# Performance work log

Hardware: AMD Instinct MI355X
Metric: run time of the kernel (lower is better)

The kernel has to match this reference:

```python
import jax, jax.numpy as jnp
import numpy as np

B, C, P, D = 4096, 1000, 10, 256
N = C * P            # total prototypes
E = 160000           # edges among prototypes
MARGIN = -0.1
LOSS_WEIGHT = 0.1
EPS = 1e-12          # F.normalize eps


def _gcn_conv(x, src, dst, deg_isqrt, w, b):
    # PyG GCNConv: symmetric-normalized aggregation with self-loops (added by caller)
    xw = x @ w                                   # [N, D]
    norm = deg_isqrt[src] * deg_isqrt[dst]       # [E+N]
    msg = norm[:, None] * xw[src]                # [E+N, D]
    out = jax.ops.segment_sum(msg, dst, num_segments=N)
    return out + b


def setup_inputs() -> dict:
    key = jax.random.key(0)
    ks = jax.random.split(key, 8)
    return {
        "hidden": jax.random.normal(ks[0], (B, D), jnp.float32),
        "labels": jax.random.randint(ks[1], (B,), 0, C),
        "edge_index": jax.random.randint(ks[2], (2, E), 0, N),
        "node_features": 0.02 * jax.random.normal(ks[3], (N, D), jnp.float32),
        "w1": jax.random.normal(ks[4], (D, D), jnp.float32) / np.sqrt(D),
        "b1": jnp.zeros((D,), jnp.float32),
        "w2": jax.random.normal(ks[5], (D, D), jnp.float32) / np.sqrt(D),
        "b2": jnp.zeros((D,), jnp.float32),
    }


def reference(hidden, labels, edge_index, node_features, w1, b1, w2, b2):
    # --- PrototypeGCN over the prototype graph (self-loops + sym norm) ---
    loops = jnp.arange(N, dtype=edge_index.dtype)
    src = jnp.concatenate([edge_index[0], loops])
    dst = jnp.concatenate([edge_index[1], loops])
    deg = jax.ops.segment_sum(jnp.ones_like(dst, jnp.float32), dst, num_segments=N)
    deg_isqrt = jnp.where(deg > 0, jax.lax.rsqrt(jnp.maximum(deg, 1.0)), 0.0)
    x = node_features
    x = jax.nn.relu(_gcn_conv(x, src, dst, deg_isqrt, w1, b1))
    x = jax.nn.relu(_gcn_conv(x, src, dst, deg_isqrt, w2, b2))

    # --- cosine similarity, per-class max over prototypes ---
    hidden_norm = hidden / jnp.maximum(jnp.linalg.norm(hidden, axis=1, keepdims=True), EPS)
    proto_norm = x / jnp.maximum(jnp.linalg.norm(x, axis=1, keepdims=True), EPS)
    sim = (1.0 + hidden_norm @ proto_norm.T) / 2.0          # [B, N]
    sim_pc = sim.reshape(B, C, P)
    output = sim_pc.max(axis=2)                              # [B, C]
    topk_idx = sim_pc.argmax(axis=2)                         # [B, C]

    # --- margin-masked cross entropy ---
    ar = jnp.arange(B)
    true_scores = output[ar, labels]
    pred_labels = output.argmax(axis=1)
    pred_scores = output.max(axis=1)
    mask = (true_scores - pred_scores) > MARGIN              # [B] bool
    cnt = mask.sum()
    per_ce = -jax.nn.log_softmax(output, axis=1)[ar, labels]
    ce_loss = jnp.sum(per_ce * mask) / jnp.maximum(cnt, 1).astype(per_ce.dtype)

    # dispersion = -mean(proto_norm @ proto_norm.T) = -||sum_i p_i||^2 / N^2
    s = proto_norm.sum(axis=0)
    dispersion_loss = -(s @ s) / (N * N)
    total_loss = jnp.where(cnt == 0, 0.0, ce_loss + LOSS_WEIGHT * dispersion_loss)

    # --- vectorized usage scatter (replaces Python double loop) ---
    pos_ids = labels * P + topk_idx[ar, labels]
    positive_usage = jnp.zeros((N,), jnp.float32).at[pos_ids].add(1.0)
    wrong = (pred_labels != labels).astype(jnp.float32)
    neg_ids = pred_labels * P + topk_idx[ar, pred_labels]
    negative_usage = jnp.zeros((N,), jnp.float32).at[neg_ids].add(wrong)

    return (output, total_loss, positive_usage, negative_usage)
```

## Files before the change

kernel.cpp:

```cpp
#include <hip/hip_runtime.h>
#include <math.h>

#define B_  4096
#define C_  1000
#define P_  10
#define D_  256
#define N_  10000
#define E_  160000

typedef __attribute__((ext_vector_type(8))) short short8;
typedef __attribute__((ext_vector_type(4))) float floatx4;

#define MFMA16(a, b, c) __builtin_amdgcn_mfma_f32_16x16x32_bf16((a), (b), (c), 0, 0, 0)

__device__ __forceinline__ float waveReduceSum(float v){
  #pragma unroll
  for (int o = 32; o > 0; o >>= 1) v += __shfl_xor(v, o);
  return v;
}
__device__ __forceinline__ unsigned short f2bf(float f){
  unsigned int u = __float_as_uint(f);
  unsigned int r = (u + 0x7FFFu + ((u >> 16) & 1u)) >> 16;
  return (unsigned short)r;
}
__device__ __forceinline__ float bf2f(unsigned short b){
  return __uint_as_float(((unsigned int)b) << 16);
}
__device__ __forceinline__ void gload_lds16(const void* g, void* l){
  __builtin_amdgcn_global_load_lds((const __attribute__((address_space(1))) void*)g,
                                   (__attribute__((address_space(3))) void*)l, 16, 0, 0);
}
__device__ __forceinline__ void split8(const float* __restrict__ p, short8& h8, short8& l8){
  float4 v0 = *(const float4*)p;
  float4 v1 = *(const float4*)(p + 4);
  float v[8] = {v0.x, v0.y, v0.z, v0.w, v1.x, v1.y, v1.z, v1.w};
  #pragma unroll
  for (int j = 0; j < 8; ++j){
    unsigned short h = f2bf(v[j]);
    h8[j] = (short)h;
    l8[j] = (short)f2bf(v[j] - bf2f(h));
  }
}

__global__ void k_prep(const int* __restrict__ src, const int* __restrict__ dst,
                       int* __restrict__ cursor, int* __restrict__ csr_src,
                       const float* __restrict__ w1, const float* __restrict__ w2,
                       unsigned short* __restrict__ w1h, unsigned short* __restrict__ w1l,
                       unsigned short* __restrict__ w2h, unsigned short* __restrict__ w2l,
                       float* __restrict__ zero_zone){
  int b = blockIdx.x;
  if (b < 625){
    int e = b * 256 + threadIdx.x;
    if (e < E_){
      int d = dst[e];
      int p = atomicAdd(&cursor[d], 1);
      p = (p < 63) ? p : 63;
      csr_src[d * 64 + p] = src[e];
    }
  } else if (b < 1137){
    int bb = b - 625;
    int k = threadIdx.x;
    const float* w = (bb < 256) ? w1 : w2;
    int n = bb & 255;
    float x = w[(size_t)k * 256 + n];
    unsigned short h = f2bf(x);
    unsigned short l = f2bf(x - bf2f(h));
    if (bb < 256){ w1h[(size_t)n * 256 + k] = h; w1l[(size_t)n * 256 + k] = l; }
    else         { w2h[(size_t)n * 256 + k] = h; w2l[(size_t)n * 256 + k] = l; }
  } else {
    int i = (b - 1137) * 256 + threadIdx.x;
    if (i < 1 + 2 * N_) zero_zone[i] = 0.f;
  }
}

__global__ __launch_bounds__(64) void k_gemm_mfma(
    const float* __restrict__ A,
    const unsigned short* __restrict__ Wh, const unsigned short* __restrict__ Wl,
    float* __restrict__ outp){
  int lane = threadIdx.x;
  int l15 = lane & 15, lq = lane >> 4;
  int rb = blockIdx.x * 64;
  int nb = blockIdx.y * 32;

  floatx4 acc[4][2];
  #pragma unroll
  for (int mt = 0; mt < 4; ++mt)
    #pragma unroll
    for (int nt = 0; nt < 2; ++nt) acc[mt][nt] = (floatx4){0.f,0.f,0.f,0.f};

  int arow[4];
  #pragma unroll
  for (int mt = 0; mt < 4; ++mt){
    int r = rb + mt * 16 + l15;
    arow[mt] = (r < N_) ? r : (N_ - 1);
  }
  for (int kc = 0; kc < 256; kc += 32){
    short8 ah[4], al[4], bh[2], bl[2];
    #pragma unroll
    for (int mt = 0; mt < 4; ++mt)
      split8(A + (size_t)arow[mt] * 256 + kc + lq * 8, ah[mt], al[mt]);
    #pragma unroll
    for (int nt = 0; nt < 2; ++nt){
      size_t o = (size_t)(nb + nt * 16 + l15) * 256 + kc + lq * 8;
      bh[nt] = *(const short8*)(Wh + o);
      bl[nt] = *(const short8*)(Wl + o);
    }
    #pragma unroll
    for (int nt = 0; nt < 2; ++nt)
      #pragma unroll
      for (int mt = 0; mt < 4; ++mt) acc[mt][nt] = MFMA16(al[mt], bh[nt], acc[mt][nt]);
    #pragma unroll
    for (int nt = 0; nt < 2; ++nt)
      #pragma unroll
      for (int mt = 0; mt < 4; ++mt) acc[mt][nt] = MFMA16(ah[mt], bl[nt], acc[mt][nt]);
    #pragma unroll
    for (int nt = 0; nt < 2; ++nt)
      #pragma unroll
      for (int mt = 0; mt < 4; ++mt) acc[mt][nt] = MFMA16(ah[mt], bh[nt], acc[mt][nt]);
  }
  #pragma unroll
  for (int mt = 0; mt < 4; ++mt)
    #pragma unroll
    for (int r = 0; r < 4; ++r){
      int row = rb + mt * 16 + lq * 4 + r;
      if (row < N_){
        #pragma unroll
        for (int nt = 0; nt < 2; ++nt)
          outp[(size_t)row * 256 + nb + nt * 16 + l15] = acc[mt][nt][r];
      }
    }
}

__global__ void k_agg_relu(const float* __restrict__ XW, const int* __restrict__ deg,
                           const int* __restrict__ csr_src,
                           const float* __restrict__ bias, float* __restrict__ X1){
  int n    = blockIdx.x * 4 + (threadIdx.x >> 6);
  int lane = threadIdx.x & 63;
  int c4   = lane * 4;
  int dgn = deg[n];
  int dg = (dgn < 64) ? dgn : 64;
  int   esr = (lane < dg) ? csr_src[n * 64 + lane] : 0;
  float is  = 1.0f / sqrtf((float)(dgn + 1));
  float en  = (1.0f / sqrtf((float)(deg[esr] + 1))) * is;
  float4 s = *(const float4*)(XW + (size_t)n * 256 + c4);
  float w = is * is;
  float4 a = make_float4(w * s.x, w * s.y, w * s.z, w * s.w);
  int i = 0;
  for (; i + 3 < dg; i += 4){
    int s0 = __shfl(esr, i),   s1 = __shfl(esr, i+1), s2 = __shfl(esr, i+2), s3 = __shfl(esr, i+3);
    float n0 = __shfl(en, i),  n1 = __shfl(en, i+1),  n2 = __shfl(en, i+2),  n3 = __shfl(en, i+3);
    float4 v0 = *(const float4*)(XW + (size_t)s0 * 256 + c4);
    float4 v1 = *(const float4*)(XW + (size_t)s1 * 256 + c4);
    float4 v2 = *(const float4*)(XW + (size_t)s2 * 256 + c4);
    float4 v3 = *(const float4*)(XW + (size_t)s3 * 256 + c4);
    a.x += n0*v0.x + n1*v1.x + n2*v2.x + n3*v3.x;
    a.y += n0*v0.y + n1*v1.y + n2*v2.y + n3*v3.y;
    a.z += n0*v0.z + n1*v1.z + n2*v2.z + n3*v3.z;
    a.w += n0*v0.w + n1*v1.w + n2*v2.w + n3*v3.w;
  }
  for (; i < dg; ++i){
    int s0 = __shfl(esr, i); float n0 = __shfl(en, i);
    float4 v0 = *(const float4*)(XW + (size_t)s0 * 256 + c4);
    a.x += n0 * v0.x; a.y += n0 * v0.y; a.z += n0 * v0.z; a.w += n0 * v0.w;
  }
  float4 b = *(const float4*)(bias + c4);
  float4 o;
  o.x = fmaxf(a.x + b.x, 0.f); o.y = fmaxf(a.y + b.y, 0.f);
  o.z = fmaxf(a.z + b.z, 0.f); o.w = fmaxf(a.w + b.w, 0.f);
  *(float4*)(X1 + (size_t)n * 256 + c4) = o;
}

__global__ void k_agg_norm_split(const float* __restrict__ XW, const int* __restrict__ deg,
                                 const int* __restrict__ csr_src,
                                 const float* __restrict__ bias,
                                 unsigned short* __restrict__ Ph, unsigned short* __restrict__ Pl){
  int n    = blockIdx.x * 4 + (threadIdx.x >> 6);
  int lane = threadIdx.x & 63;
  int c4   = lane * 4;
  int dgn = deg[n];
  int dg = (dgn < 64) ? dgn : 64;
  int   esr = (lane < dg) ? csr_src[n * 64 + lane] : 0;
  float is  = 1.0f / sqrtf((float)(dgn + 1));
  float en  = (1.0f / sqrtf((float)(deg[esr] + 1))) * is;
  float4 s = *(const float4*)(XW + (size_t)n * 256 + c4);
  float w = is * is;
  float4 a = make_float4(w * s.x, w * s.y, w * s.z, w * s.w);
  int i = 0;
  for (; i + 3 < dg; i += 4){
    int s0 = __shfl(esr, i),   s1 = __shfl(esr, i+1), s2 = __shfl(esr, i+2), s3 = __shfl(esr, i+3);
    float n0 = __shfl(en, i),  n1 = __shfl(en, i+1),  n2 = __shfl(en, i+2),  n3 = __shfl(en, i+3);
    float4 v0 = *(const float4*)(XW + (size_t)s0 * 256 + c4);
    float4 v1 = *(const float4*)(XW + (size_t)s1 * 256 + c4);
    float4 v2 = *(const float4*)(XW + (size_t)s2 * 256 + c4);
    float4 v3 = *(const float4*)(XW + (size_t)s3 * 256 + c4);
    a.x += n0*v0.x + n1*v1.x + n2*v2.x + n3*v3.x;
    a.y += n0*v0.y + n1*v1.y + n2*v2.y + n3*v3.y;
    a.z += n0*v0.z + n1*v1.z + n2*v2.z + n3*v3.z;
    a.w += n0*v0.w + n1*v1.w + n2*v2.w + n3*v3.w;
  }
  for (; i < dg; ++i){
    int s0 = __shfl(esr, i); float n0 = __shfl(en, i);
    float4 v0 = *(const float4*)(XW + (size_t)s0 * 256 + c4);
    a.x += n0 * v0.x; a.y += n0 * v0.y; a.z += n0 * v0.z; a.w += n0 * v0.w;
  }
  float4 b = *(const float4*)(bias + c4);
  float x0 = fmaxf(a.x + b.x, 0.f), x1 = fmaxf(a.y + b.y, 0.f);
  float x2 = fmaxf(a.z + b.z, 0.f), x3 = fmaxf(a.w + b.w, 0.f);
  float ss = x0*x0 + x1*x1 + x2*x2 + x3*x3;
  float tot = waveReduceSum(ss);
  float nrm = fmaxf(sqrtf(tot), 1e-12f);
  x0 /= nrm; x1 /= nrm; x2 /= nrm; x3 /= nrm;
  unsigned short h0 = f2bf(x0), h1 = f2bf(x1), h2 = f2bf(x2), h3 = f2bf(x3);
  ushort4 hv = make_ushort4(h0, h1, h2, h3);
  ushort4 lv = make_ushort4(f2bf(x0 - bf2f(h0)), f2bf(x1 - bf2f(h1)),
                            f2bf(x2 - bf2f(h2)), f2bf(x3 - bf2f(h3)));
  *(ushort4*)(Ph + (size_t)n * 256 + c4) = hv;
  *(ushort4*)(Pl + (size_t)n * 256 + c4) = lv;
}

__global__ void k_norm_split(const float* __restrict__ in,
                             unsigned short* __restrict__ hi,
                             unsigned short* __restrict__ lo,
                             const unsigned short* __restrict__ Ph,
                             const unsigned short* __restrict__ Pl,
                             float* __restrict__ svec){
  int r = blockIdx.x, t = threadIdx.x;
  if (r < B_){
    float v = in[(size_t)r * 256 + t];
    float ss = waveReduceSum(v * v);
    __shared__ float red[4];
    int w = t >> 6;
    if ((t & 63) == 0) red[w] = ss;
    __syncthreads();
    float tot = red[0] + red[1] + red[2] + red[3];
    float nrm = fmaxf(sqrtf(tot), 1e-12f);
    float x = v / nrm;
    unsigned short h = f2bf(x);
    unsigned short l = f2bf(x - bf2f(h));
    hi[(size_t)r * 256 + t] = h;
    lo[(size_t)r * 256 + t] = l;
  } else {
    int r0 = (r - B_) * 100;
    float acc = 0.f;
    for (int rr = r0; rr < r0 + 100; ++rr)
      acc += bf2f(Ph[(size_t)rr * 256 + t]) + bf2f(Pl[(size_t)rr * 256 + t]);
    atomicAdd(&svec[t], acc);
  }
}

__global__ __launch_bounds__(256, 4) void k_sim_max(
    const unsigned short* __restrict__ HNh, const unsigned short* __restrict__ HNl,
    const unsigned short* __restrict__ PNh, const unsigned short* __restrict__ PNl,
    float* __restrict__ out, unsigned char* __restrict__ idxb){
  __shared__ __align__(16) char smem[20736];

  int tid  = threadIdx.x;
  int wid  = tid >> 6;
  int lane = tid & 63;
  int l15  = lane & 15, lq = lane >> 4;
  int rbw  = blockIdx.y * 128 + wid * 32;
  int cb80 = blockIdx.x * 80;

  int swz  = (l15 >> 1) & 3;
  int srow = lane >> 2;
  int skq  = (lane & 3) ^ ((lane >> 3) & 3);

  floatx4 acc[2][5];
  #pragma unroll
  for (int mt = 0; mt < 2; ++mt)
    #pragma unroll
    for (int nt = 0; nt < 5; ++nt) acc[mt][nt] = (floatx4){0.f,0.f,0.f,0.f};

  const unsigned short* a0h = HNh + (size_t)(rbw + l15) * 256 + lq * 8;
  const unsigned short* a0l = HNl + (size_t)(rbw + l15) * 256 + lq * 8;

  auto stage1 = [&](int kc, int pb, int c){
    int bsel = (c >= 5) ? 1 : 0;
    int s = c - bsel * 5;
    int row = s * 16 + srow;
    const unsigned short* gp = (bsel ? PNl : PNh)
        + (size_t)(cb80 + row) * 256 + kc + skq * 8;
    char* lp = smem + pb * 10240 + bsel * 5120 + s * 1024;
    gload_lds16(gp, lp);
  };
  auto stageAll = [&](int kc, int pb){
    stage1(kc, pb, wid);
    stage1(kc, pb, wid + 4);
    if (wid < 2) stage1(kc, pb, wid + 8);
  };

  stageAll(0, 0);
  short8 ah[2], al[2];
  #pragma unroll
  for (int mt = 0; mt < 2; ++mt){
    ah[mt] = *(const short8*)(a0h + (size_t)mt * 4096);
    al[mt] = *(const short8*)(a0l + (size_t)mt * 4096);
  }
  __syncthreads();

  int p = 0;
  for (int kc = 0; kc < 256; kc += 32){
    const unsigned short* Bh = (const unsigned short*)(smem + p * 10240);
    const unsigned short* Bl = Bh + 2560;
    short8 ah2[2], al2[2];
    if (kc < 224){
      stageAll(kc + 32, p ^ 1);
      #pragma unroll
      for (int mt = 0; mt < 2; ++mt){
        ah2[mt] = *(const short8*)(a0h + (size_t)mt * 4096 + kc + 32);
        al2[mt] = *(const short8*)(a0l + (size_t)mt * 4096 + kc + 32);
      }
    }
    {
      int r0 = (0 * 16 + l15) * 32 + (lq ^ swz) * 8;
      int r1 = (1 * 16 + l15) * 32 + (lq ^ swz) * 8;
      int r2 = (2 * 16 + l15) * 32 + (lq ^ swz) * 8;
      short8 bh0 = *(const short8*)(Bh + r0), bl0 = *(const short8*)(Bl + r0);
      short8 bh1 = *(const short8*)(Bh + r1), bl1 = *(const short8*)(Bl + r1);
      short8 bh2 = *(const short8*)(Bh + r2), bl2 = *(const short8*)(Bl + r2);
      acc[0][0] = MFMA16(al[0], bh0, acc[0][0]);
      acc[1][0] = MFMA16(al[1], bh0, acc[1][0]);
      acc[0][1] = MFMA16(al[0], bh1, acc[0][1]);
      acc[1][1] = MFMA16(al[1], bh1, acc[1][1]);
      acc[0][2] = MFMA16(al[0], bh2, acc[0][2]);
      acc[1][2] = MFMA16(al[1], bh2, acc[1][2]);
      acc[0][0] = MFMA16(ah[0], bl0, acc[0][0]);
      acc[1][0] = MFMA16(ah[1], bl0, acc[1][0]);
      acc[0][1] = MFMA16(ah[0], bl1, acc[0][1]);
      acc[1][1] = MFMA16(ah[1], bl1, acc[1][1]);
      acc[0][2] = MFMA16(ah[0], bl2, acc[0][2]);
      acc[1][2] = MFMA16(ah[1], bl2, acc[1][2]);
      acc[0][0] = MFMA16(ah[0], bh0, acc[0][0]);
      acc[1][0] = MFMA16(ah[1], bh0, acc[1][0]);
      acc[0][1] = MFMA16(ah[0], bh1, acc[0][1]);
      acc[1][1] = MFMA16(ah[1], bh1, acc[1][1]);
      acc[0][2] = MFMA16(ah[0], bh2, acc[0][2]);
      acc[1][2] = MFMA16(ah[1], bh2, acc[1][2]);
    }
    {
      int r3 = (3 * 16 + l15) * 32 + (lq ^ swz) * 8;
      int r4 = (4 * 16 + l15) * 32 + (lq ^ swz) * 8;
      short8 bh3 = *(const short8*)(Bh + r3), bl3 = *(const short8*)(Bl + r3);
      short8 bh4 = *(const short8*)(Bh + r4), bl4 = *(const short8*)(Bl + r4);
      acc[0][3] = MFMA16(al[0], bh3, acc[0][3]);
      acc[1][3] = MFMA16(al[1], bh3, acc[1][3]);
      acc[0][4] = MFMA16(al[0], bh4, acc[0][4]);
      acc[1][4] = MFMA16(al[1], bh4, acc[1][4]);
      acc[0][3] = MFMA16(ah[0], bl3, acc[0][3]);
      acc[1][3] = MFMA16(ah[1], bl3, acc[1][3]);
      acc[0][4] = MFMA16(ah[0], bl4, acc[0][4]);
      acc[1][4] = MFMA16(ah[1], bl4, acc[1][4]);
      acc[0][3] = MFMA16(ah[0], bh3, acc[0][3]);
      acc[1][3] = MFMA16(ah[1], bh3, acc[1][3]);
      acc[0][4] = MFMA16(ah[0], bh4, acc[0][4]);
      acc[1][4] = MFMA16(ah[1], bh4, acc[1][4]);
    }
    ah[0] = ah2[0]; ah[1] = ah2[1];
    al[0] = al2[0]; al[1] = al2[1];
    __syncthreads();
    p ^= 1;
  }

  float* redw = (float*)smem + wid * 1296;
  #pragma unroll
  for (int mt = 0; mt < 2; ++mt){
    #pragma unroll
    for (int nt = 0; nt < 5; ++nt)
      #pragma unroll
      for (int r = 0; r < 4; ++r)
        redw[(lq * 4 + r) * 81 + nt * 16 + l15] = acc[mt][nt][r];
    int row = lane >> 2;
    int q   = lane & 3;
    const float* basep = redw + row * 81 + q * 20;
    float vs[2]; int is[2];
    #pragma unroll
    for (int cc = 0; cc < 2; ++cc){
      float m = 0.5f * (1.0f + basep[cc * 10]); int mi = 0;
      #pragma unroll
      for (int p2 = 1; p2 < 10; ++p2){
        float v = 0.5f * (1.0f + basep[cc * 10 + p2]);
        if (v > m){ m = v; mi = p2; }
      }
      vs[cc] = m; is[cc] = mi;
    }
    int grow = rbw + mt * 16 + row;
    int gcol = blockIdx.x * 8 + q * 2;
    *(float2*)(out + (size_t)grow * 1000 + gcol) = make_float2(vs[0], vs[1]);
    idxb[(size_t)grow * 1000 + gcol]     = (unsigned char)is[0];
    idxb[(size_t)grow * 1000 + gcol + 1] = (unsigned char)is[1];
  }
}

__global__ void k_row_pass(const float* __restrict__ out, const unsigned char* __restrict__ idxb,
                           const int* __restrict__ labels, int* __restrict__ cnt,
                           float* __restrict__ ce_sum, float* __restrict__ pos_usage,
                           float* __restrict__ neg_usage){
  int b = blockIdx.x * 4 + (threadIdx.x >> 6);
  int lane = threadIdx.x & 63;
  const float* row = out + (size_t)b * 1000;
  float m = -INFINITY, s = 0.f; int bi = 0x7fffffff;
  for (int c = lane; c < 1000; c += 64){
    float v = row[c];
    if (v > m){ s = s * expf(m - v) + 1.f; bi = c; m = v; }
    else       s += expf(v - m);
  }
  #pragma unroll
  for (int o = 32; o > 0; o >>= 1){
    float m2 = __shfl_xor(m, o);
    float s2 = __shfl_xor(s, o);
    int   b2 = __shfl_xor(bi, o);
    float M = fmaxf(m, m2);
    s = s * expf(m - M) + s2 * expf(m2 - M);
    if (m2 > m || (m2 == m && b2 < bi)) bi = b2;
    m = M;
  }
  if (lane == 0){
    int lab = labels[b];
    float true_score = row[lab];
    float per_ce = m + logf(s) - true_score;
    bool mask = (true_score - m) > -0.1f;
    if (mask){ atomicAdd(cnt, 1); atomicAdd(ce_sum, per_ce); }
    int pi = idxb[(size_t)b * 1000 + lab];
    atomicAdd(&pos_usage[lab * P_ + pi], 1.f);
    if (bi != lab){
      int ni = idxb[(size_t)b * 1000 + bi];
      atomicAdd(&neg_usage[bi * P_ + ni], 1.f);
    }
  }
}

__global__ void k_finalize(const float* __restrict__ s, const int* __restrict__ cnt,
                           const float* __restrict__ ce_sum, float* __restrict__ loss_out){
  int t = threadIdx.x;
  float v = s[t];
  float ss = waveReduceSum(v * v);
  __shared__ float red[4];
  if ((t & 63) == 0) red[t >> 6] = ss;
  __syncthreads();
  if (t == 0){
    float tot = red[0] + red[1] + red[2] + red[3];
    float disp = -tot / 1.0e8f;
    int c = *cnt;
    float total = (c == 0) ? 0.f
                : (*ce_sum / (float)(c < 1 ? 1 : c) + 0.1f * disp);
    *loss_out = total;
  }
}

extern "C" void kernel_launch(void* const* d_in, const int* in_sizes, int n_in,
                              void* d_out, int out_size, void* d_ws, size_t ws_size,
                              hipStream_t stream){
  const float* hidden = (const float*)d_in[0];
  const int*   labels = (const int*)  d_in[1];
  const int*   eidx   = (const int*)  d_in[2];
  const float* nodef  = (const float*)d_in[3];
  const float* w1     = (const float*)d_in[4];
  const float* b1     = (const float*)d_in[5];
  const float* w2     = (const float*)d_in[6];
  const float* b2     = (const float*)d_in[7];

  float* out       = (float*)d_out;
  float* loss_out  = out + (size_t)B_ * C_;
  float* pos_usage = loss_out + 1;
  float* neg_usage = pos_usage + N_;

  const int* srcp = eidx;
  const int* dstp = eidx + E_;

  char* base = (char*)d_ws;
  size_t off = 0;
  auto alloc = [&](size_t bytes) -> char* {
    char* p = base + off;
    off = (off + bytes + 255) & ~(size_t)255;
    return p;
  };
  int*   cursor  = (int*)  alloc((size_t)N_ * 4);
  float* svec    = (float*)alloc(256 * 4);
  int*   cnt     = (int*)  alloc(4);
  float* ce_sum  = (float*)alloc(4);
  size_t zero_bytes = off;
  int*   csr_src   = (int*)  alloc((size_t)N_ * 64 * 4);
  float* XW        = (float*)alloc((size_t)N_ * 256 * 4);
  float* X1        = (float*)alloc((size_t)N_ * 256 * 4);
  unsigned short* Ph  = (unsigned short*)alloc((size_t)N_ * 256 * 2);
  unsigned short* Pl  = (unsigned short*)alloc((size_t)N_ * 256 * 2);
  unsigned short* W1h = (unsigned short*)alloc(256 * 256 * 2);
  unsigned short* W1l = (unsigned short*)alloc(256 * 256 * 2);
  unsigned short* W2h = (unsigned short*)alloc(256 * 256 * 2);
  unsigned short* W2l = (unsigned short*)alloc(256 * 256 * 2);
  unsigned short* HNh = (unsigned short*)alloc((size_t)B_ * 256 * 2);
  unsigned short* HNl = (unsigned short*)alloc((size_t)B_ * 256 * 2);
  unsigned char* idxb = (unsigned char*)alloc((size_t)B_ * C_);

  hipMemsetAsync(base, 0, zero_bytes, stream);

  k_prep<<<1216, 256, 0, stream>>>(srcp, dstp, cursor, csr_src,
                                   w1, w2, W1h, W1l, W2h, W2l, loss_out);

  dim3 ggrid(157, 8);
  k_gemm_mfma<<<ggrid, 64, 0, stream>>>(nodef, W1h, W1l, XW);
  k_agg_relu<<<N_ / 4, 256, 0, stream>>>(XW, cursor, csr_src, b1, X1);
  k_gemm_mfma<<<ggrid, 64, 0, stream>>>(X1, W2h, W2l, XW);
  k_agg_norm_split<<<N_ / 4, 256, 0, stream>>>(XW, cursor, csr_src, b2, Ph, Pl);

  k_norm_split<<<B_ + 100, 256, 0, stream>>>(hidden, HNh, HNl, Ph, Pl, svec);

  dim3 sgrid(125, 32);
  k_sim_max<<<sgrid, 256, 0, stream>>>(HNh, HNl, Ph, Pl, out, idxb);

  k_row_pass<<<B_ / 4, 256, 0, stream>>>(out, idxb, labels, cnt, ce_sum, pos_usage, neg_usage);
  k_finalize<<<1, 256, 0, stream>>>(svec, cnt, ce_sum, loss_out);
}
```

Before: 340.8 us.

## Presplit GEMM inputs to bf16 hi/lo and fold small kernels into neighbors

The GEMM now loads pre-split bf16 hi/lo operands instead of splitting fp32 inside the inner loop. The first layer's node features are split in the prep kernel, and the aggregation kernel writes hi/lo directly instead of an fp32 X1. Hidden-state normalization moves into k_prep, and the prototype column sum plus the loss finalization are merged into k_row_pass using a last-block-done atomic counter. This removes two launches and the per-tile conversion work, at the cost of a much larger prep grid and an extra pass over the node features.

```diff
diff --git a/kernel.cpp b/kernel.cpp
--- a/kernel.cpp
+++ b/kernel.cpp
@@ -30,27 +30,21 @@
   __builtin_amdgcn_global_load_lds((const __attribute__((address_space(1))) void*)g,
                                    (__attribute__((address_space(3))) void*)l, 16, 0, 0);
 }
-__device__ __forceinline__ void split8(const float* __restrict__ p, short8& h8, short8& l8){
-  float4 v0 = *(const float4*)p;
-  float4 v1 = *(const float4*)(p + 4);
-  float v[8] = {v0.x, v0.y, v0.z, v0.w, v1.x, v1.y, v1.z, v1.w};
-  #pragma unroll
-  for (int j = 0; j < 8; ++j){
-    unsigned short h = f2bf(v[j]);
-    h8[j] = (short)h;
-    l8[j] = (short)f2bf(v[j] - bf2f(h));
-  }
-}
 
 __global__ void k_prep(const int* __restrict__ src, const int* __restrict__ dst,
                        int* __restrict__ cursor, int* __restrict__ csr_src,
                        const float* __restrict__ w1, const float* __restrict__ w2,
                        unsigned short* __restrict__ w1h, unsigned short* __restrict__ w1l,
                        unsigned short* __restrict__ w2h, unsigned short* __restrict__ w2l,
-                       float* __restrict__ zero_zone){
+                       float* __restrict__ zero_zone,
+                       const float* __restrict__ nodef,
+                       unsigned short* __restrict__ NFh, unsigned short* __restrict__ NFl,
+                       const float* __restrict__ hidden,
+                       unsigned short* __restrict__ HNh, unsigned short* __restrict__ HNl){
   int b = blockIdx.x;
+  int t = threadIdx.x;
   if (b < 625){
-    int e = b * 256 + threadIdx.x;
+    int e = b * 256 + t;
     if (e < E_){
       int d = dst[e];
       int p = atomicAdd(&cursor[d], 1);
@@ -59,22 +53,41 @@
     }
   } else if (b < 1137){
     int bb = b - 625;
-    int k = threadIdx.x;
     const float* w = (bb < 256) ? w1 : w2;
     int n = bb & 255;
-    float x = w[(size_t)k * 256 + n];
+    float x = w[(size_t)t * 256 + n];
     unsigned short h = f2bf(x);
     unsigned short l = f2bf(x - bf2f(h));
-    if (bb < 256){ w1h[(size_t)n * 256 + k] = h; w1l[(size_t)n * 256 + k] = l; }
-    else         { w2h[(size_t)n * 256 + k] = h; w2l[(size_t)n * 256 + k] = l; }
+    if (bb < 256){ w1h[(size_t)n * 256 + t] = h; w1l[(size_t)n * 256 + t] = l; }
+    else         { w2h[(size_t)n * 256 + t] = h; w2l[(size_t)n * 256 + t] = l; }
+  } else if (b < 1216){
+    int i = (b - 1137) * 256 + t;
+    if (i < 1 + 2 * N_) zero_zone[i] = 0.f;
+  } else if (b < 11216){
+    size_t i = (size_t)(b - 1216) * 256 + t;
+    float x = nodef[i];
+    unsigned short h = f2bf(x);
+    NFh[i] = h;
+    NFl[i] = f2bf(x - bf2f(h));
   } else {
-    int i = (b - 1137) * 256 + threadIdx.x;
-    if (i < 1 + 2 * N_) zero_zone[i] = 0.f;
+    int r = b - 11216;
+    float v = hidden[(size_t)r * 256 + t];
+    float ss = waveReduceSum(v * v);
+    __shared__ float red[4];
+    int w = t >> 6;
+    if ((t & 63) == 0) red[w] = ss;
+    __syncthreads();
+    float tot = red[0] + red[1] + red[2] + red[3];
+    float nrm = fmaxf(sqrtf(tot), 1e-12f);
+    float x = v / nrm;
+    unsigned short h = f2bf(x);
+    HNh[(size_t)r * 256 + t] = h;
+    HNl[(size_t)r * 256 + t] = f2bf(x - bf2f(h));
   }
 }
 
 __global__ __launch_bounds__(64) void k_gemm_mfma(
-    const float* __restrict__ A,
+    const unsigned short* __restrict__ Ah, const unsigned short* __restrict__ Al,
     const unsigned short* __restrict__ Wh, const unsigned short* __restrict__ Wl,
     float* __restrict__ outp){
   int lane = threadIdx.x;
@@ -97,8 +110,11 @@
   for (int kc = 0; kc < 256; kc += 32){
     short8 ah[4], al[4], bh[2], bl[2];
     #pragma unroll
-    for (int mt = 0; mt < 4; ++mt)
-      split8(A + (size_t)arow[mt] * 256 + kc + lq * 8, ah[mt], al[mt]);
+    for (int mt = 0; mt < 4; ++mt){
+      size_t o = (size_t)arow[mt] * 256 + kc + lq * 8;
+      ah[mt] = *(const short8*)(Ah + o);
+      al[mt] = *(const short8*)(Al + o);
+    }
     #pragma unroll
     for (int nt = 0; nt < 2; ++nt){
       size_t o = (size_t)(nb + nt * 16 + l15) * 256 + kc + lq * 8;
@@ -131,9 +147,10 @@
     }
 }
 
-__global__ void k_agg_relu(const float* __restrict__ XW, const int* __restrict__ deg,
-                           const int* __restrict__ csr_src,
-                           const float* __restrict__ bias, float* __restrict__ X1){
+__global__ void k_agg_split(const float* __restrict__ XW, const int* __restrict__ deg,
+                            const int* __restrict__ csr_src,
+                            const float* __restrict__ bias,
+                            unsigned short* __restrict__ Xh, unsigned short* __restrict__ Xl){
   int n    = blockIdx.x * 4 + (threadIdx.x >> 6);
   int lane = threadIdx.x & 63;
   int c4   = lane * 4;
@@ -164,10 +181,14 @@
     a.x += n0 * v0.x; a.y += n0 * v0.y; a.z += n0 * v0.z; a.w += n0 * v0.w;
   }
   float4 b = *(const float4*)(bias + c4);
-  float4 o;
-  o.x = fmaxf(a.x + b.x, 0.f); o.y = fmaxf(a.y + b.y, 0.f);
-  o.z = fmaxf(a.z + b.z, 0.f); o.w = fmaxf(a.w + b.w, 0.f);
-  *(float4*)(X1 + (size_t)n * 256 + c4) = o;
+  float x0 = fmaxf(a.x + b.x, 0.f), x1 = fmaxf(a.y + b.y, 0.f);
+  float x2 = fmaxf(a.z + b.z, 0.f), x3 = fmaxf(a.w + b.w, 0.f);
+  unsigned short h0 = f2bf(x0), h1 = f2bf(x1), h2 = f2bf(x2), h3 = f2bf(x3);
+  ushort4 hv = make_ushort4(h0, h1, h2, h3);
+  ushort4 lv = make_ushort4(f2bf(x0 - bf2f(h0)), f2bf(x1 - bf2f(h1)),
+                            f2bf(x2 - bf2f(h2)), f2bf(x3 - bf2f(h3)));
+  *(ushort4*)(Xh + (size_t)n * 256 + c4) = hv;
+  *(ushort4*)(Xl + (size_t)n * 256 + c4) = lv;
 }
 
 __global__ void k_agg_norm_split(const float* __restrict__ XW, const int* __restrict__ deg,
@@ -218,36 +239,6 @@
   *(ushort4*)(Pl + (size_t)n * 256 + c4) = lv;
 }
 
-__global__ void k_norm_split(const float* __restrict__ in,
-                             unsigned short* __restrict__ hi,
-                             unsigned short* __restrict__ lo,
-                             const unsigned short* __restrict__ Ph,
-                             const unsigned short* __restrict__ Pl,
-                             float* __restrict__ svec){
-  int r = blockIdx.x, t = threadIdx.x;
-  if (r < B_){
-    float v = in[(size_t)r * 256 + t];
-    float ss = waveReduceSum(v * v);
-    __shared__ float red[4];
-    int w = t >> 6;
-    if ((t & 63) == 0) red[w] = ss;
-    __syncthreads();
-    float tot = red[0] + red[1] + red[2] + red[3];
-    float nrm = fmaxf(sqrtf(tot), 1e-12f);
-    float x = v / nrm;
-    unsigned short h = f2bf(x);
-    unsigned short l = f2bf(x - bf2f(h));
-    hi[(size_t)r * 256 + t] = h;
-    lo[(size_t)r * 256 + t] = l;
-  } else {
-    int r0 = (r - B_) * 100;
-    float acc = 0.f;
-    for (int rr = r0; rr < r0 + 100; ++rr)
-      acc += bf2f(Ph[(size_t)rr * 256 + t]) + bf2f(Pl[(size_t)rr * 256 + t]);
-    atomicAdd(&svec[t], acc);
-  }
-}
-
 __global__ __launch_bounds__(256, 4) void k_sim_max(
     const unsigned short* __restrict__ HNh, const unsigned short* __restrict__ HNl,
     const unsigned short* __restrict__ PNh, const unsigned short* __restrict__ PNl,
@@ -394,56 +385,78 @@
 __global__ void k_row_pass(const float* __restrict__ out, const unsigned char* __restrict__ idxb,
                            const int* __restrict__ labels, int* __restrict__ cnt,
                            float* __restrict__ ce_sum, float* __restrict__ pos_usage,
-                           float* __restrict__ neg_usage){
-  int b = blockIdx.x * 4 + (threadIdx.x >> 6);
-  int lane = threadIdx.x & 63;
-  const float* row = out + (size_t)b * 1000;
-  float m = -INFINITY, s = 0.f; int bi = 0x7fffffff;
-  for (int c = lane; c < 1000; c += 64){
-    float v = row[c];
-    if (v > m){ s = s * expf(m - v) + 1.f; bi = c; m = v; }
-    else       s += expf(v - m);
-  }
-  #pragma unroll
-  for (int o = 32; o > 0; o >>= 1){
-    float m2 = __shfl_xor(m, o);
-    float s2 = __shfl_xor(s, o);
-    int   b2 = __shfl_xor(bi, o);
-    float M = fmaxf(m, m2);
-    s = s * expf(m - M) + s2 * expf(m2 - M);
-    if (m2 > m || (m2 == m && b2 < bi)) bi = b2;
-    m = M;
-  }
-  if (lane == 0){
-    int lab = labels[b];
-    float true_score = row[lab];
-    float per_ce = m + logf(s) - true_score;
-    bool mask = (true_score - m) > -0.1f;
-    if (mask){ atomicAdd(cnt, 1); atomicAdd(ce_sum, per_ce); }
-    int pi = idxb[(size_t)b * 1000 + lab];
-    atomicAdd(&pos_usage[lab * P_ + pi], 1.f);
-    if (bi != lab){
-      int ni = idxb[(size_t)b * 1000 + bi];
-      atomicAdd(&neg_usage[bi * P_ + ni], 1.f);
-    }
-  }
-}
-
-__global__ void k_finalize(const float* __restrict__ s, const int* __restrict__ cnt,
-                           const float* __restrict__ ce_sum, float* __restrict__ loss_out){
-  int t = threadIdx.x;
-  float v = s[t];
-  float ss = waveReduceSum(v * v);
-  __shared__ float red[4];
-  if ((t & 63) == 0) red[t >> 6] = ss;
+                           float* __restrict__ neg_usage,
+                           const unsigned short* __restrict__ Ph,
+                           const unsigned short* __restrict__ Pl,
+                           float* __restrict__ svec, int* __restrict__ done,
+                           float* __restrict__ loss_out){
+  int blk = blockIdx.x;
+  if (blk < 1024){
+    int b = blk * 4 + (threadIdx.x >> 6);
+    int lane = threadIdx.x & 63;
+    const float* row = out + (size_t)b * 1000;
+    float m = -INFINITY, s = 0.f; int bi = 0x7fffffff;
+    for (int c = lane; c < 1000; c += 64){
+      float v = row[c];
+      if (v > m){ s = s * expf(m - v) + 1.f; bi = c; m = v; }
+      else       s += expf(v - m);
+    }
+    #pragma unroll
+    for (int o = 32; o > 0; o >>= 1){
+      float m2 = __shfl_xor(m, o);
+      float s2 = __shfl_xor(s, o);
+      int   b2 = __shfl_xor(bi, o);
+      float M = fmaxf(m, m2);
+      s = s * expf(m - M) + s2 * expf(m2 - M);
+      if (m2 > m || (m2 == m && b2 < bi)) bi = b2;
+      m = M;
+    }
+    if (lane == 0){
+      int lab = labels[b];
+      float true_score = row[lab];
+      float per_ce = m + logf(s) - true_score;
+      bool mask = (true_score - m) > -0.1f;
+      if (mask){ atomicAdd(cnt, 1); atomicAdd(ce_sum, per_ce); }
+      int pi = idxb[(size_t)b * 1000 + lab];
+      atomicAdd(&pos_usage[lab * P_ + pi], 1.f);
+      if (bi != lab){
+        int ni = idxb[(size_t)b * 1000 + bi];
+        atomicAdd(&neg_usage[bi * P_ + ni], 1.f);
+      }
+    }
+  } else {
+    int t = threadIdx.x;
+    int r0 = (blk - 1024) * 100;
+    float acc = 0.f;
+    for (int rr = r0; rr < r0 + 100; ++rr)
+      acc += bf2f(Ph[(size_t)rr * 256 + t]) + bf2f(Pl[(size_t)rr * 256 + t]);
+    atomicAdd(&svec[t], acc);
+  }
+  __threadfence();
   __syncthreads();
-  if (t == 0){
-    float tot = red[0] + red[1] + red[2] + red[3];
-    float disp = -tot / 1.0e8f;
-    int c = *cnt;
-    float total = (c == 0) ? 0.f
-                : (*ce_sum / (float)(c < 1 ? 1 : c) + 0.1f * disp);
-    *loss_out = total;
+  __shared__ int last;
+  if (threadIdx.x == 0){
+    int d = atomicAdd(done, 1);
+    last = (d == 1124 - 1) ? 1 : 0;
+  }
+  __syncthreads();
+  if (last){
+    __threadfence();
+    int t = threadIdx.x;
+    float v = atomicAdd(&svec[t], 0.f);
+    float ss = waveReduceSum(v * v);
+    __shared__ float red[4];
+    if ((t & 63) == 0) red[t >> 6] = ss;
+    __syncthreads();
+    if (t == 0){
+      float tot = red[0] + red[1] + red[2] + red[3];
+      float disp = -tot / 1.0e8f;
+      int c = atomicAdd(cnt, 0);
+      float ces = atomicAdd(ce_sum, 0.f);
+      float total = (c == 0) ? 0.f
+                  : (ces / (float)(c < 1 ? 1 : c) + 0.1f * disp);
+      *loss_out = total;
+    }
   }
 }
 
@@ -478,10 +491,14 @@
   float* svec    = (float*)alloc(256 * 4);
   int*   cnt     = (int*)  alloc(4);
   float* ce_sum  = (float*)alloc(4);
+  int*   done    = (int*)  alloc(4);
   size_t zero_bytes = off;
   int*   csr_src   = (int*)  alloc((size_t)N_ * 64 * 4);
   float* XW        = (float*)alloc((size_t)N_ * 256 * 4);
-  float* X1        = (float*)alloc((size_t)N_ * 256 * 4);
+  unsigned short* NFh = (unsigned short*)alloc((size_t)N_ * 256 * 2);
+  unsigned short* NFl = (unsigned short*)alloc((size_t)N_ * 256 * 2);
+  unsigned short* Xh  = (unsigned short*)alloc((size_t)N_ * 256 * 2);
+  unsigned short* Xl  = (unsigned short*)alloc((size_t)N_ * 256 * 2);
   unsigned short* Ph  = (unsigned short*)alloc((size_t)N_ * 256 * 2);
   unsigned short* Pl  = (unsigned short*)alloc((size_t)N_ * 256 * 2);
   unsigned short* W1h = (unsigned short*)alloc(256 * 256 * 2);
@@ -494,20 +511,19 @@
 
   hipMemsetAsync(base, 0, zero_bytes, stream);
 
-  k_prep<<<1216, 256, 0, stream>>>(srcp, dstp, cursor, csr_src,
-                                   w1, w2, W1h, W1l, W2h, W2l, loss_out);
+  k_prep<<<15312, 256, 0, stream>>>(srcp, dstp, cursor, csr_src,
+                                    w1, w2, W1h, W1l, W2h, W2l, loss_out,
+                                    nodef, NFh, NFl, hidden, HNh, HNl);
 
   dim3 ggrid(157, 8);
-  k_gemm_mfma<<<ggrid, 64, 0, stream>>>(nodef, W1h, W1l, XW);
-  k_agg_relu<<<N_ / 4, 256, 0, stream>>>(XW, cursor, csr_src, b1, X1);
-  k_gemm_mfma<<<ggrid, 64, 0, stream>>>(X1, W2h, W2l, XW);
+  k_gemm_mfma<<<ggrid, 64, 0, stream>>>(NFh, NFl, W1h, W1l, XW);
+  k_agg_split<<<N_ / 4, 256, 0, stream>>>(XW, cursor, csr_src, b1, Xh, Xl);
+  k_gemm_mfma<<<ggrid, 64, 0, stream>>>(Xh, Xl, W2h, W2l, XW);
   k_agg_norm_split<<<N_ / 4, 256, 0, stream>>>(XW, cursor, csr_src, b2, Ph, Pl);
-
-  k_norm_split<<<B_ + 100, 256, 0, stream>>>(hidden, HNh, HNl, Ph, Pl, svec);
 
   dim3 sgrid(125, 32);
   k_sim_max<<<sgrid, 256, 0, stream>>>(HNh, HNl, Ph, Pl, out, idxb);
 
-  k_row_pass<<<B_ / 4, 256, 0, stream>>>(out, idxb, labels, cnt, ce_sum, pos_usage, neg_usage);
-  k_finalize<<<1, 256, 0, stream>>>(svec, cnt, ce_sum, loss_out);
-}
+  k_row_pass<<<1124, 256, 0, stream>>>(out, idxb, labels, cnt, ce_sum,
+                                       pos_usage, neg_usage, Ph, Pl, svec, done, loss_out);
+}
```

New measurement: 383.3 us. 12.5% more time.
